# Kernel optimization log

Hardware: AMD Instinct MI355X
Metric: run time of the kernel (lower is better)

The kernel has to match this reference:

```python
import jax, jax.numpy as jnp
import numpy as np

B, T, D = 4, 2048, 2048
N_HEADS, N_KV = 16, 4
HEAD_DIM = D // N_HEADS  # 128
N_REP = N_HEADS // N_KV
THETA = 10000.0


def _rope_cos_sin(seq_len, dim, theta):
    inv_freq = 1.0 / (theta ** (jnp.arange(0, dim, 2, dtype=jnp.float32) / dim))
    t = jnp.arange(seq_len, dtype=jnp.float32)
    freqs = jnp.outer(t, inv_freq)               # [T, dim/2]
    emb = jnp.concatenate([freqs, freqs], -1)    # [T, dim]
    return jnp.cos(emb)[None, None], jnp.sin(emb)[None, None]  # [1,1,T,dim]


def _rotate_half(x):
    x1, x2 = jnp.split(x, 2, axis=-1)
    return jnp.concatenate([-x2, x1], axis=-1)


def setup_inputs() -> dict:
    key = jax.random.key(0)
    ks = jax.random.split(key, 5)
    x = jax.random.normal(ks[0], (B, T, D), dtype=jnp.float32)
    # additive causal mask
    causal = jnp.tril(jnp.ones((T, T), dtype=bool))
    mask = jnp.where(causal, 0.0, -1e9).astype(jnp.float32)[None, None]
    s = 0.02
    wq = jax.random.normal(ks[1], (D, N_HEADS * HEAD_DIM), dtype=jnp.float32) * s
    wk = jax.random.normal(ks[2], (D, N_KV * HEAD_DIM), dtype=jnp.float32) * s
    wv = jax.random.normal(ks[3], (D, N_KV * HEAD_DIM), dtype=jnp.float32) * s
    wo = jax.random.normal(ks[4], (D, D), dtype=jnp.float32) * s
    return {"x": x, "mask": mask, "wq": wq, "wk": wk, "wv": wv, "wo": wo}


def reference(x, mask, wq, wk, wv, wo):
    Bc, Tc, _ = x.shape
    q = (x @ wq).reshape(Bc, Tc, N_HEADS, HEAD_DIM).transpose(0, 2, 1, 3)  # [B,H,T,hd]
    k = (x @ wk).reshape(Bc, Tc, N_KV, HEAD_DIM).transpose(0, 2, 1, 3)     # [B,Kv,T,hd]
    v = (x @ wv).reshape(Bc, Tc, N_KV, HEAD_DIM).transpose(0, 2, 1, 3)

    cos, sin = _rope_cos_sin(Tc, HEAD_DIM, THETA)
    q = q * cos + _rotate_half(q) * sin
    k = k * cos + _rotate_half(k) * sin

    # repeat kv heads: [B,Kv,T,hd] -> [B,Kv*n_rep,T,hd]
    k = jnp.repeat(k, N_REP, axis=1)
    v = jnp.repeat(v, N_REP, axis=1)

    scale = HEAD_DIM ** -0.5
    attn = jnp.einsum("bhqd,bhkd->bhqk", q, k) * scale
    attn = attn + mask
    attn = jax.nn.softmax(attn, axis=-1)
    out = jnp.einsum("bhqk,bhkd->bhqd", attn, v)  # [B,H,T,hd]
    out = out.transpose(0, 2, 1, 3).reshape(Bc, Tc, -1)
    return out @ wo
```

## Files before the change

### kernel.cpp

```cpp
#include <hip/hip_runtime.h>

typedef __bf16 bf16;
typedef float  f32x4  __attribute__((ext_vector_type(4)));
typedef float  f32x2  __attribute__((ext_vector_type(2)));
typedef __bf16 bf16x8 __attribute__((ext_vector_type(8)));
typedef __bf16 bf16x4 __attribute__((ext_vector_type(4)));
typedef unsigned short ushort4_ __attribute__((ext_vector_type(4)));

typedef unsigned int __attribute__((address_space(1))) uint_g;
typedef unsigned int __attribute__((address_space(3))) uint_l;

#define DEV __device__ __forceinline__

DEV void gload16(const void* g, void* l) {
  __builtin_amdgcn_global_load_lds((uint_g*)g, (uint_l*)l, 16, 0, 0);
}

#define PHASE_SYNC do { \
  asm volatile("s_barrier" ::: "memory"); \
  asm volatile("s_waitcnt lgkmcnt(0)" ::: "memory"); \
  __builtin_amdgcn_sched_barrier(0); } while (0)

__global__ void k_cvt(const float* __restrict__ in, bf16* __restrict__ out) {
  int i = blockIdx.x * 256 + threadIdx.x;
  f32x4 v = *((const f32x4*)in + i);
  bf16x4 o;
  o[0] = (bf16)v[0]; o[1] = (bf16)v[1]; o[2] = (bf16)v[2]; o[3] = (bf16)v[3];
  *((bf16x4*)out + i) = o;
}

__global__ void k_transpose_cvt(const float* __restrict__ in, bf16* __restrict__ out,
                                int K, int N) {
  __shared__ bf16 tile[64][65];
  int n0 = blockIdx.x * 64, k0 = blockIdx.y * 64;
  int tx = threadIdx.x & 63, ty = threadIdx.x >> 6;
#pragma unroll
  for (int r = 0; r < 64; r += 4)
    tile[r + ty][tx] = (bf16)in[(size_t)(k0 + r + ty) * N + n0 + tx];
  __syncthreads();
#pragma unroll
  for (int r = 0; r < 64; r += 4)
    out[(size_t)(n0 + r + ty) * K + k0 + tx] = tile[tx][r + ty];
}

__global__ void k_rope_tab(f32x2* __restrict__ tab) {
  int idx = blockIdx.x * 256 + threadIdx.x;
  int t = idx >> 6, i = idx & 63;
  float inv = powf(10000.f, -(float)i * (1.f / 64.f));
  float ang = (float)t * inv;
  f32x2 cs; cs[0] = cosf(ang); cs[1] = sinf(ang);
  tab[idx] = cs;
}

template <int MODE>
__global__ __launch_bounds__(512, 2) void k_gemm256(const bf16* __restrict__ A,
                                                    const bf16* __restrict__ Bt,
                                                    void* __restrict__ Cq,
                                                    bf16* __restrict__ Ck,
                                                    bf16* __restrict__ Cv,
                                                    int K) {
  __shared__ bf16 Asm[2][256 * 64];
  __shared__ bf16 Bsm[2][256 * 64];
  const int tid = threadIdx.x;
  const int w = tid >> 6, l = tid & 63, lr = l & 15, lg = l >> 4;
  const int wr = w >> 2, wc = w & 3;
  const int bn = blockIdx.x, bm = blockIdx.y;

  const int srow = tid >> 3;
  const int scb = ((tid & 7) << 4) ^ ((srow & 7) << 4);
  const bf16* Ag = A  + ((size_t)(bm * 256) + srow) * K;
  const bf16* Bg = Bt + ((size_t)(bn * 256) + srow) * K;
  const int ldsbase = w << 10;

  auto stA = [&](int buf, int s, int k0) {
    gload16((const char*)Ag + ((size_t)(s * 64) * K + k0) * 2 + scb,
            (char*)&Asm[buf][0] + s * 8192 + ldsbase);
  };
  auto stB = [&](int buf, int s, int k0) {
    gload16((const char*)Bg + ((size_t)(s * 64) * K + k0) * 2 + scb,
            (char*)&Bsm[buf][0] + s * 8192 + ldsbase);
  };
  auto ldA = [&](int buf, int mf, int kk) -> bf16x8 {
    int row = wr * 128 + mf * 16 + lr;
    return *(const bf16x8*)((const char*)&Asm[buf][0] + row * 128 +
                            ((kk * 64 + lg * 16) ^ ((lr & 7) << 4)));
  };
  auto ldB = [&](int buf, int nf, int kk) -> bf16x8 {
    int row = wc * 64 + nf * 16 + lr;
    return *(const bf16x8*)((const char*)&Bsm[buf][0] + row * 128 +
                            ((kk * 64 + lg * 16) ^ ((lr & 7) << 4)));
  };

  f32x4 acc[8][4] = {};
  const int nt = K >> 6;

#pragma unroll
  for (int s = 0; s < 4; s++) { stA(0, s, 0); stB(0, s, 0); }
  asm volatile("s_waitcnt vmcnt(0)" ::: "memory");
  __syncthreads();

#pragma unroll 1
  for (int t = 0; t < nt; t++) {
    const int cur = t & 1, nxt = cur ^ 1;
    const int kn = (t + 1) << 6;
    const bool pre = (t + 1 < nt);
    bf16x8 a0[4][2], a1[4][2], b0[2][2], b1[2][2];

#pragma unroll
    for (int mf = 0; mf < 4; mf++) { a0[mf][0] = ldA(cur, mf, 0); a0[mf][1] = ldA(cur, mf, 1); }
#pragma unroll
    for (int nf = 0; nf < 2; nf++) { b0[nf][0] = ldB(cur, nf, 0); b0[nf][1] = ldB(cur, nf, 1); }
    if (pre) { stA(nxt, 0, kn); stA(nxt, 1, kn); stA(nxt, 2, kn); }
    PHASE_SYNC;
    __builtin_amdgcn_s_setprio(1);
#pragma unroll
    for (int mf = 0; mf < 4; mf++)
#pragma unroll
      for (int nf = 0; nf < 2; nf++)
#pragma unroll
        for (int kk = 0; kk < 2; kk++)
          acc[mf][nf] = __builtin_amdgcn_mfma_f32_16x16x32_bf16(a0[mf][kk], b0[nf][kk], acc[mf][nf], 0, 0, 0);
    __builtin_amdgcn_s_setprio(0);

#pragma unroll
    for (int nf = 0; nf < 2; nf++) { b1[nf][0] = ldB(cur, nf + 2, 0); b1[nf][1] = ldB(cur, nf + 2, 1); }
    if (pre) { stA(nxt, 3, kn); stB(nxt, 0, kn); stB(nxt, 1, kn); }
    PHASE_SYNC;
    __builtin_amdgcn_s_setprio(1);
#pragma unroll
    for (int mf = 0; mf < 4; mf++)
#pragma unroll
      for (int nf = 0; nf < 2; nf++)
#pragma unroll
        for (int kk = 0; kk < 2; kk++)
          acc[mf][nf + 2] = __builtin_amdgcn_mfma_f32_16x16x32_bf16(a0[mf][kk], b1[nf][kk], acc[mf][nf + 2], 0, 0, 0);
    __builtin_amdgcn_s_setprio(0);

#pragma unroll
    for (int mf = 0; mf < 4; mf++) { a1[mf][0] = ldA(cur, mf + 4, 0); a1[mf][1] = ldA(cur, mf + 4, 1); }
#pragma unroll
    for (int nf = 0; nf < 2; nf++) { b0[nf][0] = ldB(cur, nf, 0); b0[nf][1] = ldB(cur, nf, 1); }
    if (pre) { stB(nxt, 2, kn); stB(nxt, 3, kn); }
    PHASE_SYNC;
    __builtin_amdgcn_s_setprio(1);
#pragma unroll
    for (int mf = 0; mf < 4; mf++)
#pragma unroll
      for (int nf = 0; nf < 2; nf++)
#pragma unroll
        for (int kk = 0; kk < 2; kk++)
          acc[mf + 4][nf] = __builtin_amdgcn_mfma_f32_16x16x32_bf16(a1[mf][kk], b0[nf][kk], acc[mf + 4][nf], 0, 0, 0);
    __builtin_amdgcn_s_setprio(0);

    __builtin_amdgcn_s_setprio(1);
#pragma unroll
    for (int mf = 0; mf < 4; mf++)
#pragma unroll
      for (int nf = 0; nf < 2; nf++)
#pragma unroll
        for (int kk = 0; kk < 2; kk++)
          acc[mf + 4][nf + 2] = __builtin_amdgcn_mfma_f32_16x16x32_bf16(a1[mf][kk], b1[nf][kk], acc[mf + 4][nf + 2], 0, 0, 0);
    __builtin_amdgcn_s_setprio(0);
    asm volatile("s_waitcnt vmcnt(0)" ::: "memory");
    asm volatile("s_barrier" ::: "memory");
  }

#pragma unroll
  for (int mf = 0; mf < 8; mf++) {
    const int rowb = bm * 256 + wr * 128 + mf * 16 + lg * 4;
#pragma unroll
    for (int nf = 0; nf < 4; nf++) {
      const int col = bn * 256 + wc * 64 + nf * 16 + lr;
      if constexpr (MODE == 0) {
        float* Cf = (float*)Cq;
#pragma unroll
        for (int j = 0; j < 4; j++)
          Cf[(size_t)(rowb + j) * 2048 + col] = acc[mf][nf][j];
      } else {
        if (bn < 8) {
          bf16* Cb = (bf16*)Cq;
#pragma unroll
          for (int j = 0; j < 4; j++)
            Cb[(size_t)(rowb + j) * 2048 + col] = (bf16)acc[mf][nf][j];
        } else if (bn < 10) {
          int kcol = col - 2048;
#pragma unroll
          for (int j = 0; j < 4; j++)
            Ck[(size_t)(rowb + j) * 512 + kcol] = (bf16)acc[mf][nf][j];
        } else {
          int vcol = col - 2560;
          int kv = vcol >> 7, d = vcol & 127;
          int bb = rowb >> 11, t0 = rowb & 2047;
          size_t off = ((size_t)((bb * 4 + kv) * 128 + d)) * 2048 + t0;
          ushort4_ pk;
#pragma unroll
          for (int j = 0; j < 4; j++)
            pk[j] = __builtin_bit_cast(unsigned short, (bf16)acc[mf][nf][j]);
          *(ushort4_*)(Cv + off) = pk;
        }
      }
    }
  }
}

template <int LOGNH>
__global__ void k_rope(const bf16* __restrict__ in, bf16* __restrict__ out,
                       const f32x2* __restrict__ tab) {
  const int NH = 1 << LOGNH;
  int idx = blockIdx.x * 256 + threadIdx.x;
  int dq = idx & 15;
  int h = (idx >> 4) & (NH - 1);
  int bt = idx >> (4 + LOGNH);
  int t = bt & 2047;
  int d0 = dq * 4;
  const bf16* pin = in + (size_t)bt * (NH * 128) + h * 128;
  bf16x4 x1 = *(const bf16x4*)(pin + d0);
  bf16x4 x2 = *(const bf16x4*)(pin + 64 + d0);
  bf16x4 o1, o2;
#pragma unroll
  for (int j = 0; j < 4; j++) {
    f32x2 cs = tab[t * 64 + d0 + j];
    float a = (float)x1[j], c2 = (float)x2[j];
    o1[j] = (bf16)(a * cs[0] - c2 * cs[1]);
    o2[j] = (bf16)(c2 * cs[0] + a * cs[1]);
  }
  int b = bt >> 11;
  bf16* pout = out + (((size_t)(b << LOGNH) + h) * 2048 + t) * 128;
  *(bf16x4*)(pout + d0) = o1;
  *(bf16x4*)(pout + 64 + d0) = o2;
}

__global__ __launch_bounds__(256, 2) void k_attn(const bf16* __restrict__ Qb,
                                                 const bf16* __restrict__ Kb,
                                                 const bf16* __restrict__ Vt,
                                                 bf16* __restrict__ AO) {
  __shared__ bf16 Ks[2][64 * 128];
  __shared__ bf16 Vs[128 * 64];
  __shared__ bf16 Ps[4][32 * 64];
  const int tid = threadIdx.x, w = tid >> 6, l = tid & 63;
  const int bh = blockIdx.y, b = bh >> 4, h = bh & 15, kvh = h >> 2;
  const int pi = blockIdx.x;
  const int lr = l & 15, lg = l >> 4;
  const float cc = 0.08838834764831845f * 1.4426950408889634f;

  const bf16* Kh = Kb + (size_t)(b * 4 + kvh) * (2048 * 128);
  const bf16* Vh = Vt + (size_t)(b * 4 + kvh) * (128 * 2048);
  char* Pw = (char*)&Ps[w][0];

  auto stageV = [&](int kv0) {
#pragma unroll
    for (int i = 0; i < 4; i++) {
      int vrow = w * 32 + i * 8 + (l >> 3);
      int vcb = ((l & 7) * 16) ^ ((vrow & 7) << 4);
      gload16(Vh + (size_t)vrow * 2048 + kv0 + (vcb >> 1), (bf16*)Vs + w * 2048 + i * 512);
    }
  };
  auto stageK = [&](int kv0, int buf) {
#pragma unroll
    for (int i = 0; i < 4; i++) {
      int krow = w * 16 + i * 4 + lg;
      int kcb = ((l & 15) * 16) ^ ((krow & 7) << 4);
      gload16(Kh + (size_t)(kv0 + krow) * 128 + (kcb >> 1), &Ks[buf][w * 2048 + i * 512]);
    }
  };

#pragma unroll 1
  for (int ph = 0; ph < 2; ph++) {
    const int q0 = (ph ? (15 - pi) : pi) * 128;
    const int nt = q0 / 64 + 2;
    const int qmaxw = q0 + w * 32 + 31;

    bf16x8 qf[2][4];
#pragma unroll
    for (int nq = 0; nq < 2; nq++) {
      const bf16* qp = Qb + (((size_t)(b * 16 + h) * 2048) + q0 + w * 32 + nq * 16 + lr) * 128 + lg * 8;
#pragma unroll
      for (int kk = 0; kk < 4; kk++) qf[nq][kk] = *(const bf16x8*)(qp + kk * 32);
    }

    f32x4 ot[8][2] = {};
    float m_[2] = {-1e30f, -1e30f}, l_[2] = {0.f, 0.f};

    int cur = 0;
    stageK(0, 0);
    __syncthreads();

#pragma unroll 1
    for (int t = 0; t < nt; t++) {
      const int kv0 = t * 64;
      stageV(kv0);
      if (t + 1 < nt) stageK(kv0 + 64, cur ^ 1);
      const bool act = (kv0 <= qmaxw);

      if (act) {
        f32x4 st[4][2] = {};
        __builtin_amdgcn_s_setprio(1);
#pragma unroll
        for (int kk = 0; kk < 4; kk++) {
#pragma unroll
          for (int nb = 0; nb < 4; nb++) {
            int row = nb * 16 + lr;
            const char* p = (const char*)&Ks[cur][0] + row * 256 + ((kk * 64 + lg * 16) ^ ((lr & 7) << 4));
            bf16x8 kf = *(const bf16x8*)p;
#pragma unroll
            for (int nq = 0; nq < 2; nq++)
              st[nb][nq] = __builtin_amdgcn_mfma_f32_16x16x32_bf16(kf, qf[nq][kk], st[nb][nq], 0, 0, 0);
          }
        }
        __builtin_amdgcn_s_setprio(0);

        const bool needmask = (kv0 + 63 > q0 + w * 32);
        float pv[2][4][4], pmax[2];
#pragma unroll
        for (int nq = 0; nq < 2; nq++) {
          const int qg = q0 + w * 32 + nq * 16 + lr;
          float mx = -1e30f;
#pragma unroll
          for (int nb = 0; nb < 4; nb++)
#pragma unroll
            for (int j = 0; j < 4; j++) {
              float v = st[nb][nq][j];
              if (needmask) {
                int kg = kv0 + nb * 16 + lg * 4 + j;
                if (kg > qg) v = -1e30f;
              }
              pv[nq][nb][j] = v;
              mx = fmaxf(mx, v);
            }
          pmax[nq] = mx;
        }
        if (!__all(fmaxf(pmax[0] - m_[0], pmax[1] - m_[1]) <= 64.f)) {
          float corr[2];
#pragma unroll
          for (int nq = 0; nq < 2; nq++) {
            float mx = pmax[nq];
            mx = fmaxf(mx, __shfl_xor(mx, 16));
            mx = fmaxf(mx, __shfl_xor(mx, 32));
            float mnew = fmaxf(m_[nq], mx);
            corr[nq] = exp2f((m_[nq] - mnew) * cc);
            m_[nq] = mnew;
            l_[nq] *= corr[nq];
          }
#pragma unroll
          for (int df = 0; df < 8; df++)
#pragma unroll
            for (int nq = 0; nq < 2; nq++)
              ot[df][nq] *= corr[nq];
        }
#pragma unroll
        for (int nq = 0; nq < 2; nq++) {
          float ls = 0.f;
#pragma unroll
          for (int nb = 0; nb < 4; nb++)
#pragma unroll
            for (int j = 0; j < 4; j++) {
              float pe = exp2f((pv[nq][nb][j] - m_[nq]) * cc);
              pv[nq][nb][j] = pe;
              ls += pe;
            }
          ls += __shfl_xor(ls, 16);
          ls += __shfl_xor(ls, 32);
          l_[nq] += ls;
          const int qloc = nq * 16 + lr;
#pragma unroll
          for (int nb = 0; nb < 4; nb++) {
            ushort4_ pk;
#pragma unroll
            for (int j = 0; j < 4; j++)
              pk[j] = __builtin_bit_cast(unsigned short, (bf16)pv[nq][nb][j]);
            *(ushort4_*)(Pw + qloc * 128 + ((nb * 32 + lg * 8) ^ ((qloc & 7) << 4))) = pk;
          }
        }
      }

      __syncthreads();

      if (act) {
        __builtin_amdgcn_s_setprio(1);
#pragma unroll
        for (int s = 0; s < 2; s++) {
          bf16x8 pf[2];
#pragma unroll
          for (int nq = 0; nq < 2; nq++) {
            int qloc = nq * 16 + lr;
            pf[nq] = *(const bf16x8*)(Pw + qloc * 128 + ((s * 64 + lg * 16) ^ ((qloc & 7) << 4)));
          }
#pragma unroll
          for (int df = 0; df < 8; df++) {
            int vrow = df * 16 + lr;
            const char* vp = (const char*)Vs + vrow * 128 + ((s * 64 + lg * 16) ^ ((vrow & 7) << 4));
            bf16x8 vf = *(const bf16x8*)vp;
#pragma unroll
            for (int nq = 0; nq < 2; nq++)
              ot[df][nq] = __builtin_amdgcn_mfma_f32_16x16x32_bf16(vf, pf[nq], ot[df][nq], 0, 0, 0);
          }
        }
        __builtin_amdgcn_s_setprio(0);
      }

      __syncthreads();
      cur ^= 1;
    }

#pragma unroll
    for (int nq = 0; nq < 2; nq++) {
      float inv = 1.f / l_[nq];
      int qg = q0 + w * 32 + nq * 16 + lr;
      bf16* op = AO + ((size_t)b * 2048 + qg) * 2048 + h * 128;
#pragma unroll
      for (int df = 0; df < 8; df++) {
        ushort4_ pk;
#pragma unroll
        for (int j = 0; j < 4; j++)
          pk[j] = __builtin_bit_cast(unsigned short, (bf16)(ot[df][nq][j] * inv));
        *(ushort4_*)(op + df * 16 + lg * 4) = pk;
      }
    }
  }
}

extern "C" void kernel_launch(void* const* d_in, const int* in_sizes, int n_in,
                              void* d_out, int out_size, void* d_ws, size_t ws_size,
                              hipStream_t stream) {
  const float* x  = (const float*)d_in[0];
  const float* wq = (const float*)d_in[2];
  const float* wk = (const float*)d_in[3];
  const float* wv = (const float*)d_in[4];
  const float* wo = (const float*)d_in[5];

  char* p = (char*)d_ws;
  auto alloc = [&](size_t bytes) { char* r = p; p += (bytes + 255) & ~(size_t)255; return r; };
  bf16*  xb     = (bf16*)alloc(8192ull * 2048 * 2);
  bf16*  wqkvT  = (bf16*)alloc(3072ull * 2048 * 2);
  bf16*  woT    = (bf16*)alloc(2048ull * 2048 * 2);
  f32x2* tab    = (f32x2*)alloc(2048ull * 64 * 8);
  bf16*  Qtmp   = (bf16*)alloc(8192ull * 2048 * 2);
  bf16*  Ktmp   = (bf16*)alloc(8192ull * 512 * 2);
  bf16*  Qr     = (bf16*)alloc(8192ull * 2048 * 2);
  bf16*  Kr     = (bf16*)alloc(8192ull * 512 * 2);
  bf16*  Vr     = (bf16*)alloc(8192ull * 512 * 2);

  k_cvt<<<16384, 256, 0, stream>>>(x, xb);
  k_transpose_cvt<<<dim3(32, 32), 256, 0, stream>>>(wq, wqkvT, 2048, 2048);
  k_transpose_cvt<<<dim3(8, 32),  256, 0, stream>>>(wk, wqkvT + 2048ull * 2048, 2048, 512);
  k_transpose_cvt<<<dim3(8, 32),  256, 0, stream>>>(wv, wqkvT + 2560ull * 2048, 2048, 512);
  k_transpose_cvt<<<dim3(32, 32), 256, 0, stream>>>(wo, woT, 2048, 2048);
  k_rope_tab<<<512, 256, 0, stream>>>(tab);

  k_gemm256<1><<<dim3(12, 32), 512, 0, stream>>>(xb, wqkvT, Qtmp, Ktmp, Vr, 2048);

  k_rope<4><<<8192, 256, 0, stream>>>(Qtmp, Qr, tab);
  k_rope<2><<<2048, 256, 0, stream>>>(Ktmp, Kr, tab);

  k_attn<<<dim3(8, 64), 256, 0, stream>>>(Qr, Kr, Vr, Qtmp);

  k_gemm256<0><<<dim3(8, 32), 512, 0, stream>>>(Qtmp, woT, d_out, nullptr, nullptr, 2048);
}
```

Baseline: 367.5 us.

## Rework attention kernel with 32x32 MFMA, single-tile blocks and folded softmax scale

Rewrites the attention kernel to use 32x32x16 MFMA tiles, so each wave holds 32 query rows in one accumulator layout. Blocks now handle a single query tile instead of a paired causal tile, doubling the grid and raising the occupancy hint to 3. The K double buffer is dropped and K and V are staged together behind one barrier. The softmax scale and log2(e) are folded into Q during RoPE, which removes per-element multiplies and tightens the lazy rescale threshold. Costs: causal load balancing across blocks is lost and K loads no longer overlap compute, while the lower per-block LDS use allows more resident blocks.

Result: slower. 445.3 us (+21.2%).

```diff
diff --git a/kernel.cpp b/kernel.cpp
--- a/kernel.cpp
+++ b/kernel.cpp
@@ -3,9 +3,11 @@
 typedef __bf16 bf16;
 typedef float  f32x4  __attribute__((ext_vector_type(4)));
 typedef float  f32x2  __attribute__((ext_vector_type(2)));
+typedef float  f32x16 __attribute__((ext_vector_type(16)));
 typedef __bf16 bf16x8 __attribute__((ext_vector_type(8)));
 typedef __bf16 bf16x4 __attribute__((ext_vector_type(4)));
 typedef unsigned short ushort4_ __attribute__((ext_vector_type(4)));
+typedef unsigned int   uint2_   __attribute__((ext_vector_type(2)));
 
 typedef unsigned int __attribute__((address_space(1))) uint_g;
 typedef unsigned int __attribute__((address_space(3))) uint_l;
@@ -205,7 +207,7 @@
 
 template <int LOGNH>
 __global__ void k_rope(const bf16* __restrict__ in, bf16* __restrict__ out,
-                       const f32x2* __restrict__ tab) {
+                       const f32x2* __restrict__ tab, float scl) {
   const int NH = 1 << LOGNH;
   int idx = blockIdx.x * 256 + threadIdx.x;
   int dq = idx & 15;
@@ -220,9 +222,10 @@
 #pragma unroll
   for (int j = 0; j < 4; j++) {
     f32x2 cs = tab[t * 64 + d0 + j];
+    float c1 = cs[0] * scl, s1 = cs[1] * scl;
     float a = (float)x1[j], c2 = (float)x2[j];
-    o1[j] = (bf16)(a * cs[0] - c2 * cs[1]);
-    o2[j] = (bf16)(c2 * cs[0] + a * cs[1]);
+    o1[j] = (bf16)(a * c1 - c2 * s1);
+    o2[j] = (bf16)(c2 * c1 + a * s1);
   }
   int b = bt >> 11;
   bf16* pout = out + (((size_t)(b << LOGNH) + h) * 2048 + t) * 128;
@@ -230,193 +233,140 @@
   *(bf16x4*)(pout + 64 + d0) = o2;
 }
 
-__global__ __launch_bounds__(256, 2) void k_attn(const bf16* __restrict__ Qb,
+__global__ __launch_bounds__(256, 3) void k_attn(const bf16* __restrict__ Qb,
                                                  const bf16* __restrict__ Kb,
                                                  const bf16* __restrict__ Vt,
                                                  bf16* __restrict__ AO) {
-  __shared__ bf16 Ks[2][64 * 128];
+  __shared__ bf16 Ks[64 * 128];
   __shared__ bf16 Vs[128 * 64];
   __shared__ bf16 Ps[4][32 * 64];
   const int tid = threadIdx.x, w = tid >> 6, l = tid & 63;
   const int bh = blockIdx.y, b = bh >> 4, h = bh & 15, kvh = h >> 2;
-  const int pi = blockIdx.x;
-  const int lr = l & 15, lg = l >> 4;
-  const float cc = 0.08838834764831845f * 1.4426950408889634f;
+  const int q0 = (15 - blockIdx.x) * 128;
+  const int l31 = l & 31, hi = l >> 5;
 
   const bf16* Kh = Kb + (size_t)(b * 4 + kvh) * (2048 * 128);
   const bf16* Vh = Vt + (size_t)(b * 4 + kvh) * (128 * 2048);
-  char* Pw = (char*)&Ps[w][0];
-
-  auto stageV = [&](int kv0) {
+
+  const int qg = q0 + w * 32 + l31;
+  bf16x8 qf[8];
+  {
+    const bf16* qp = Qb + (((size_t)(b * 16 + h) * 2048) + qg) * 128 + hi * 8;
+#pragma unroll
+    for (int kk = 0; kk < 8; kk++) qf[kk] = *(const bf16x8*)(qp + kk * 16);
+  }
+
+  f32x16 ot[4] = {};
+  float m_ = -3e38f, l_ = 0.f;
+  const int qw0 = q0 + w * 32;
+  const int nt = q0 / 64 + 2;
+  char* Pw = (char*)&Ps[w][0] + l31 * 128;
+  const int qsw = (l & 7) << 4;
+
+#pragma unroll 1
+  for (int t = 0; t < nt; t++) {
+    const int kv0 = t * 64;
 #pragma unroll
     for (int i = 0; i < 4; i++) {
+      int krow = w * 16 + i * 4 + (l >> 4);
+      int kcb = ((l & 15) * 16) ^ ((krow & 7) << 4);
+      gload16(Kh + (size_t)(kv0 + krow) * 128 + (kcb >> 1), (bf16*)Ks + w * 2048 + i * 512);
       int vrow = w * 32 + i * 8 + (l >> 3);
       int vcb = ((l & 7) * 16) ^ ((vrow & 7) << 4);
       gload16(Vh + (size_t)vrow * 2048 + kv0 + (vcb >> 1), (bf16*)Vs + w * 2048 + i * 512);
     }
-  };
-  auto stageK = [&](int kv0, int buf) {
-#pragma unroll
-    for (int i = 0; i < 4; i++) {
-      int krow = w * 16 + i * 4 + lg;
-      int kcb = ((l & 15) * 16) ^ ((krow & 7) << 4);
-      gload16(Kh + (size_t)(kv0 + krow) * 128 + (kcb >> 1), &Ks[buf][w * 2048 + i * 512]);
-    }
-  };
-
-#pragma unroll 1
-  for (int ph = 0; ph < 2; ph++) {
-    const int q0 = (ph ? (15 - pi) : pi) * 128;
-    const int nt = q0 / 64 + 2;
-    const int qmaxw = q0 + w * 32 + 31;
-
-    bf16x8 qf[2][4];
-#pragma unroll
-    for (int nq = 0; nq < 2; nq++) {
-      const bf16* qp = Qb + (((size_t)(b * 16 + h) * 2048) + q0 + w * 32 + nq * 16 + lr) * 128 + lg * 8;
-#pragma unroll
-      for (int kk = 0; kk < 4; kk++) qf[nq][kk] = *(const bf16x8*)(qp + kk * 32);
-    }
-
-    f32x4 ot[8][2] = {};
-    float m_[2] = {-1e30f, -1e30f}, l_[2] = {0.f, 0.f};
-
-    int cur = 0;
-    stageK(0, 0);
     __syncthreads();
 
-#pragma unroll 1
-    for (int t = 0; t < nt; t++) {
-      const int kv0 = t * 64;
-      stageV(kv0);
-      if (t + 1 < nt) stageK(kv0 + 64, cur ^ 1);
-      const bool act = (kv0 <= qmaxw);
-
-      if (act) {
-        f32x4 st[4][2] = {};
-        __builtin_amdgcn_s_setprio(1);
-#pragma unroll
-        for (int kk = 0; kk < 4; kk++) {
-#pragma unroll
-          for (int nb = 0; nb < 4; nb++) {
-            int row = nb * 16 + lr;
-            const char* p = (const char*)&Ks[cur][0] + row * 256 + ((kk * 64 + lg * 16) ^ ((lr & 7) << 4));
-            bf16x8 kf = *(const bf16x8*)p;
-#pragma unroll
-            for (int nq = 0; nq < 2; nq++)
-              st[nb][nq] = __builtin_amdgcn_mfma_f32_16x16x32_bf16(kf, qf[nq][kk], st[nb][nq], 0, 0, 0);
-          }
+    if (kv0 <= qw0 + 31) {
+      f32x16 st[2] = {};
+      __builtin_amdgcn_s_setprio(1);
+#pragma unroll
+      for (int nb = 0; nb < 2; nb++) {
+        const int row = nb * 32 + l31;
+        const char* kbase = (const char*)Ks + row * 256;
+#pragma unroll
+        for (int kk = 0; kk < 8; kk++) {
+          bf16x8 kf = *(const bf16x8*)(kbase + ((kk * 32 + hi * 16) ^ qsw));
+          st[nb] = __builtin_amdgcn_mfma_f32_32x32x16_bf16(kf, qf[kk], st[nb], 0, 0, 0);
         }
-        __builtin_amdgcn_s_setprio(0);
-
-        const bool needmask = (kv0 + 63 > q0 + w * 32);
-        float pv[2][4][4], pmax[2];
-#pragma unroll
-        for (int nq = 0; nq < 2; nq++) {
-          const int qg = q0 + w * 32 + nq * 16 + lr;
-          float mx = -1e30f;
-#pragma unroll
-          for (int nb = 0; nb < 4; nb++)
-#pragma unroll
-            for (int j = 0; j < 4; j++) {
-              float v = st[nb][nq][j];
-              if (needmask) {
-                int kg = kv0 + nb * 16 + lg * 4 + j;
-                if (kg > qg) v = -1e30f;
-              }
-              pv[nq][nb][j] = v;
-              mx = fmaxf(mx, v);
-            }
-          pmax[nq] = mx;
-        }
-        if (!__all(fmaxf(pmax[0] - m_[0], pmax[1] - m_[1]) <= 64.f)) {
-          float corr[2];
-#pragma unroll
-          for (int nq = 0; nq < 2; nq++) {
-            float mx = pmax[nq];
-            mx = fmaxf(mx, __shfl_xor(mx, 16));
-            mx = fmaxf(mx, __shfl_xor(mx, 32));
-            float mnew = fmaxf(m_[nq], mx);
-            corr[nq] = exp2f((m_[nq] - mnew) * cc);
-            m_[nq] = mnew;
-            l_[nq] *= corr[nq];
-          }
-#pragma unroll
-          for (int df = 0; df < 8; df++)
-#pragma unroll
-            for (int nq = 0; nq < 2; nq++)
-              ot[df][nq] *= corr[nq];
-        }
-#pragma unroll
-        for (int nq = 0; nq < 2; nq++) {
-          float ls = 0.f;
-#pragma unroll
-          for (int nb = 0; nb < 4; nb++)
-#pragma unroll
-            for (int j = 0; j < 4; j++) {
-              float pe = exp2f((pv[nq][nb][j] - m_[nq]) * cc);
-              pv[nq][nb][j] = pe;
-              ls += pe;
-            }
-          ls += __shfl_xor(ls, 16);
-          ls += __shfl_xor(ls, 32);
-          l_[nq] += ls;
-          const int qloc = nq * 16 + lr;
-#pragma unroll
-          for (int nb = 0; nb < 4; nb++) {
-            ushort4_ pk;
-#pragma unroll
-            for (int j = 0; j < 4; j++)
-              pk[j] = __builtin_bit_cast(unsigned short, (bf16)pv[nq][nb][j]);
-            *(ushort4_*)(Pw + qloc * 128 + ((nb * 32 + lg * 8) ^ ((qloc & 7) << 4))) = pk;
+      }
+      __builtin_amdgcn_s_setprio(0);
+
+      if (kv0 + 63 > qw0) {
+#pragma unroll
+        for (int nb = 0; nb < 2; nb++) {
+          const int kvb = kv0 + nb * 32 + 4 * hi;
+#pragma unroll
+          for (int r = 0; r < 16; r++) {
+            int kg = kvb + (r & 3) + 8 * (r >> 2);
+            if (kg > qg) st[nb][r] = -3e38f;
           }
         }
       }
-
-      __syncthreads();
-
-      if (act) {
-        __builtin_amdgcn_s_setprio(1);
-#pragma unroll
-        for (int s = 0; s < 2; s++) {
-          bf16x8 pf[2];
-#pragma unroll
-          for (int nq = 0; nq < 2; nq++) {
-            int qloc = nq * 16 + lr;
-            pf[nq] = *(const bf16x8*)(Pw + qloc * 128 + ((s * 64 + lg * 16) ^ ((qloc & 7) << 4)));
+      float mx = -3e38f;
+#pragma unroll
+      for (int nb = 0; nb < 2; nb++)
+#pragma unroll
+        for (int r = 0; r < 16; r++) mx = fmaxf(mx, st[nb][r]);
+      mx = fmaxf(mx, __shfl_xor(mx, 32));
+      if (!__all(mx - m_ <= 8.f)) {
+        float mnew = fmaxf(m_, mx);
+        float corr = exp2f(m_ - mnew);
+        m_ = mnew; l_ *= corr;
+#pragma unroll
+        for (int dt = 0; dt < 4; dt++)
+#pragma unroll
+          for (int r = 0; r < 16; r++) ot[dt][r] *= corr;
+      }
+      float ls = 0.f;
+#pragma unroll
+      for (int nb = 0; nb < 2; nb++)
+#pragma unroll
+        for (int a = 0; a < 4; a++) {
+          uint2_ pr;
+#pragma unroll
+          for (int half = 0; half < 2; half++) {
+            float p0 = exp2f(st[nb][4 * a + 2 * half] - m_);
+            float p1 = exp2f(st[nb][4 * a + 2 * half + 1] - m_);
+            ls += p0 + p1;
+            unsigned short b0 = __builtin_bit_cast(unsigned short, (bf16)p0);
+            unsigned short b1 = __builtin_bit_cast(unsigned short, (bf16)p1);
+            pr[half] = (unsigned int)b0 | ((unsigned int)b1 << 16);
           }
-#pragma unroll
-          for (int df = 0; df < 8; df++) {
-            int vrow = df * 16 + lr;
-            const char* vp = (const char*)Vs + vrow * 128 + ((s * 64 + lg * 16) ^ ((vrow & 7) << 4));
-            bf16x8 vf = *(const bf16x8*)vp;
-#pragma unroll
-            for (int nq = 0; nq < 2; nq++)
-              ot[df][nq] = __builtin_amdgcn_mfma_f32_16x16x32_bf16(vf, pf[nq], ot[df][nq], 0, 0, 0);
-          }
+          *(uint2_*)(Pw + ((nb * 64 + a * 16 + hi * 8) ^ qsw)) = pr;
         }
-        __builtin_amdgcn_s_setprio(0);
+      ls += __shfl_xor(ls, 32);
+      l_ += ls;
+
+      __builtin_amdgcn_s_setprio(1);
+#pragma unroll
+      for (int kb = 0; kb < 4; kb++) {
+        bf16x8 pb = *(const bf16x8*)(Pw + ((kb * 32 + hi * 16) ^ qsw));
+#pragma unroll
+        for (int dt = 0; dt < 4; dt++) {
+          const int vrow = dt * 32 + l31;
+          const char* vp = (const char*)Vs + vrow * 128 + ((kb * 32 + hi * 16) ^ qsw);
+          bf16x8 vf = *(const bf16x8*)vp;
+          ot[dt] = __builtin_amdgcn_mfma_f32_32x32x16_bf16(vf, pb, ot[dt], 0, 0, 0);
+        }
       }
-
-      __syncthreads();
-      cur ^= 1;
+      __builtin_amdgcn_s_setprio(0);
     }
-
-#pragma unroll
-    for (int nq = 0; nq < 2; nq++) {
-      float inv = 1.f / l_[nq];
-      int qg = q0 + w * 32 + nq * 16 + lr;
-      bf16* op = AO + ((size_t)b * 2048 + qg) * 2048 + h * 128;
-#pragma unroll
-      for (int df = 0; df < 8; df++) {
-        ushort4_ pk;
-#pragma unroll
-        for (int j = 0; j < 4; j++)
-          pk[j] = __builtin_bit_cast(unsigned short, (bf16)(ot[df][nq][j] * inv));
-        *(ushort4_*)(op + df * 16 + lg * 4) = pk;
-      }
+    __syncthreads();
+  }
+
+  const float inv = 1.f / l_;
+  bf16* op = AO + ((size_t)b * 2048 + qg) * 2048 + h * 128;
+#pragma unroll
+  for (int dt = 0; dt < 4; dt++)
+#pragma unroll
+    for (int rq = 0; rq < 4; rq++) {
+      ushort4_ pk;
+#pragma unroll
+      for (int j = 0; j < 4; j++)
+        pk[j] = __builtin_bit_cast(unsigned short, (bf16)(ot[dt][rq * 4 + j] * inv));
+      *(ushort4_*)(op + dt * 32 + rq * 8 + hi * 4) = pk;
     }
-  }
 }
 
 extern "C" void kernel_launch(void* const* d_in, const int* in_sizes, int n_in,
@@ -449,10 +399,11 @@
 
   k_gemm256<1><<<dim3(12, 32), 512, 0, stream>>>(xb, wqkvT, Qtmp, Ktmp, Vr, 2048);
 
-  k_rope<4><<<8192, 256, 0, stream>>>(Qtmp, Qr, tab);
-  k_rope<2><<<2048, 256, 0, stream>>>(Ktmp, Kr, tab);
-
-  k_attn<<<dim3(8, 64), 256, 0, stream>>>(Qr, Kr, Vr, Qtmp);
+  const float qscl = 0.08838834764831845f * 1.4426950408889634f;
+  k_rope<4><<<8192, 256, 0, stream>>>(Qtmp, Qr, tab, qscl);
+  k_rope<2><<<2048, 256, 0, stream>>>(Ktmp, Kr, tab, 1.0f);
+
+  k_attn<<<dim3(16, 64), 256, 0, stream>>>(Qr, Kr, Vr, Qtmp);
 
   k_gemm256<0><<<dim3(8, 32), 512, 0, stream>>>(Qtmp, woT, d_out, nullptr, nullptr, 2048);
 }
```
